# Optimization experiments

Hardware: AMD Instinct MI355X
Metric: run time of the kernel (lower is better)

Reference implementation:

```python
import jax, jax.numpy as jnp
import numpy as np

D_MODEL = 512
D_FF = 512
N_EXPERTS = 16
TOP_K = 3
BATCH, SEQ = 1, 2048


def setup_inputs() -> dict:
    key = jax.random.key(0)
    ks = jax.random.split(key, 6)
    x = jax.random.normal(ks[0], (BATCH, SEQ, D_MODEL), dtype=jnp.float32)
    # router gate (std=0.01 per _init_weights)
    gate_w = 0.01 * jax.random.normal(ks[1], (N_EXPERTS, D_MODEL), dtype=jnp.float32)
    expert_bias = jnp.zeros((N_EXPERTS,), dtype=jnp.float32)  # registered buffer, zeros
    # shared SwiGLU expert (std=0.02)
    shared_gate_up = 0.02 * jax.random.normal(ks[2], (2 * D_FF, D_MODEL), dtype=jnp.float32)
    shared_down = 0.02 * jax.random.normal(ks[3], (D_MODEL, D_FF), dtype=jnp.float32)
    # batched routed experts (std=0.02)
    expert_gate_up = 0.02 * jax.random.normal(ks[4], (N_EXPERTS, 2 * D_FF, D_MODEL), dtype=jnp.float32)
    expert_down = 0.02 * jax.random.normal(ks[5], (N_EXPERTS, D_MODEL, D_FF), dtype=jnp.float32)
    return {
        "x": x,
        "gate_w": gate_w,
        "expert_bias": expert_bias,
        "shared_gate_up": shared_gate_up,
        "shared_down": shared_down,
        "expert_gate_up": expert_gate_up,
        "expert_down": expert_down,
    }


def _swiglu(combined):
    gate, up = jnp.split(combined, 2, axis=-1)
    return jax.nn.silu(gate) * up


def reference(x, gate_w, expert_bias, shared_gate_up, shared_down, expert_gate_up, expert_down):
    B, S, D = x.shape
    xf = x.reshape(-1, D)  # [T, D]

    # ---- shared expert (always active) ----
    shared_out = _swiglu(xf @ shared_gate_up.T) @ shared_down.T  # [T, D]

    # ---- router: sigmoid affinity + bias-adjusted top-k ----
    logits = xf @ gate_w.T  # [T, E]
    affinity = jax.nn.sigmoid(logits)
    routing_scores = affinity + expert_bias  # expert_bias buffer (zeros)
    _, sel = jax.lax.top_k(routing_scores, TOP_K)  # [T, K]
    sel_aff = jnp.take_along_axis(affinity, sel, axis=1)  # [T, K]
    gating = sel_aff / (sel_aff.sum(axis=-1, keepdims=True) + 1e-9)  # [T, K]

    # ---- routed experts: per-token SwiGLU with the token's expert weights ----
    # Computed densely per expert then gathered; identical math to the
    # per-token weight-gather in BatchedExperts.
    combined = jnp.einsum('td,efd->tef', xf, expert_gate_up)  # [T, E, 2F]
    hidden = _swiglu(combined)  # [T, E, F]
    expert_out = jnp.einsum('tef,edf->ted', hidden, expert_down)  # [T, E, D]
    sel_out = jnp.take_along_axis(expert_out, sel[:, :, None], axis=1)  # [T, K, D]
    routed_out = jnp.einsum('tk,tkd->td', gating, sel_out)  # [T, D]

    out = shared_out + routed_out  # dropout p=0.0 -> identity
    return out.reshape(B, S, D)
```

## Files before the change

### kernel.cpp

```cpp
#include <hip/hip_runtime.h>

#define T_TOK 2048
#define DM    512
#define DFF   512
#define NE    16
#define LDK   72

typedef __attribute__((ext_vector_type(8))) short bf16x8;
typedef __attribute__((ext_vector_type(4))) float f32x4;
typedef __attribute__((ext_vector_type(8))) unsigned short us8;

__device__ __forceinline__ unsigned short f2bf(float f) {
  unsigned int u = __float_as_uint(f);
  u += 0x7fffu + ((u >> 16) & 1u);
  return (unsigned short)(u >> 16);
}

#define MFMA(a,b,c) __builtin_amdgcn_mfma_f32_16x16x32_bf16((a),(b),(c),0,0,0)

__global__ __launch_bounds__(256) void prep_kernel(
    const float* __restrict__ x, const float* __restrict__ gw,
    const float* __restrict__ bias, int* __restrict__ counts,
    int* __restrict__ list, float* __restrict__ wgt,
    const float* __restrict__ sgu, const float* __restrict__ sdn,
    const float* __restrict__ egu, const float* __restrict__ edn,
    unsigned short* __restrict__ xb,   unsigned short* __restrict__ sgub,
    unsigned short* __restrict__ sdnb, unsigned short* __restrict__ egub,
    unsigned short* __restrict__ ednb)
{
  const int tid = threadIdx.x;
  if (blockIdx.x >= 512) {
    int g = (blockIdx.x - 512) * 256 + tid;
    const float* s; unsigned short* d; int l;
    if      (g <  131072) { s = x;   d = xb;   l = g;           }
    else if (g <  196608) { s = sgu; d = sgub; l = g -  131072; }
    else if (g <  229376) { s = sdn; d = sdnb; l = g -  196608; }
    else if (g < 1277952) { s = egu; d = egub; l = g -  229376; }
    else                  { s = edn; d = ednb; l = g - 1277952; }
    const float* p = s + (size_t)l * 8;
    float4 v0 = *(const float4*)p;
    float4 v1 = *(const float4*)(p + 4);
    us8 o;
    o[0]=f2bf(v0.x); o[1]=f2bf(v0.y); o[2]=f2bf(v0.z); o[3]=f2bf(v0.w);
    o[4]=f2bf(v1.x); o[5]=f2bf(v1.y); o[6]=f2bf(v1.z); o[7]=f2bf(v1.w);
    *(us8*)(d + (size_t)l * 8) = o;
    return;
  }

  __shared__ float lg[4][16];
  __shared__ int bcnt[16], bbase[16];
  __shared__ int sel_s[4][3], pos_s[4][3];
  __shared__ float g_s[4][3];

  const int w = tid >> 6, lane = tid & 63;
  if (tid < 16) bcnt[tid] = 0;
  const int tok = blockIdx.x * 4 + w;
  const int e = lane & 15, part = lane >> 4;

  const float* xr = x + (size_t)tok * DM + part * 128;
  const float* wr = gw + (size_t)e * DM + part * 128;
  float acc = 0.f;
  #pragma unroll 8
  for (int i = 0; i < 128; i += 4) {
    float4 xv = *(const float4*)(xr + i);
    float4 wv = *(const float4*)(wr + i);
    acc += xv.x*wv.x + xv.y*wv.y + xv.z*wv.z + xv.w*wv.w;
  }
  acc += __shfl_xor(acc, 16);
  acc += __shfl_xor(acc, 32);
  if (lane < 16) lg[w][lane] = 1.f / (1.f + __expf(-acc));
  __syncthreads();

  if (tid < 4) {
    float aff[16], sc[16];
    #pragma unroll
    for (int i = 0; i < 16; ++i) { aff[i] = lg[tid][i]; sc[i] = aff[i] + bias[i]; }
    int sel[3]; float sa[3]; float sum = 0.f;
    #pragma unroll
    for (int k = 0; k < 3; ++k) {
      float best = -1e30f; int bi = 0;
      for (int i = 0; i < 16; ++i) {
        bool used = false;
        for (int j = 0; j < k; ++j) used |= (sel[j] == i);
        if (!used && sc[i] > best) { best = sc[i]; bi = i; }
      }
      sel[k] = bi; sa[k] = aff[bi]; sum += aff[bi];
    }
    float inv = 1.f / (sum + 1e-9f);
    #pragma unroll
    for (int k = 0; k < 3; ++k) {
      int p = atomicAdd(&bcnt[sel[k]], 1);
      sel_s[tid][k] = sel[k]; pos_s[tid][k] = p; g_s[tid][k] = sa[k] * inv;
    }
  }
  __syncthreads();
  if (tid < 16) bbase[tid] = atomicAdd(&counts[tid], bcnt[tid]);
  __syncthreads();
  if (tid < 4) {
    #pragma unroll
    for (int k = 0; k < 3; ++k) {
      int E = sel_s[tid][k];
      int p = bbase[E] + pos_s[tid][k];
      list[E * T_TOK + p] = blockIdx.x * 4 + tid;
      wgt [E * T_TOK + p] = g_s[tid][k];
    }
  }
}

__global__ __launch_bounds__(256, 4) void gemm1_fused(
    const unsigned short* __restrict__ X, const unsigned short* __restrict__ Wsh,
    const unsigned short* __restrict__ Wex, unsigned short* __restrict__ Hall,
    const int* __restrict__ counts, const int* __restrict__ list)
{
  __shared__ unsigned short As[64][LDK];
  __shared__ unsigned short Bg[64][LDK];
  __shared__ unsigned short Bu[64][LDK];

  const int n0 = blockIdx.x * 64;
  const int mt = blockIdx.y, z = blockIdx.z;
  int cnt, hb; const unsigned short* W;
  if (z == 0) { cnt = T_TOK; hb = 0; W = Wsh; }
  else {
    const int e = z - 1;
    cnt = counts[e];
    if (mt * 64 >= cnt) return;
    hb = T_TOK;
    for (int i = 0; i < e; ++i) hb += counts[i];
    W = Wex + (size_t)e * (2 * DFF * DM);
  }

  const int tid = threadIdx.x;
  const int sr = tid >> 2;
  const int sc = (tid & 3) * 16;
  const int entry = mt * 64 + sr;
  const bool avalid = entry < cnt;
  const unsigned short* arow = X;
  if (avalid) {
    const int tok = (z == 0) ? entry : list[(z - 1) * T_TOK + entry];
    arow = X + (size_t)tok * DM;
  }
  const unsigned short* grow = W + (size_t)(n0 + sr) * DM;
  const unsigned short* urow = W + (size_t)(DFF + n0 + sr) * DM;

  const int lane = tid & 63;
  const int wm = ((tid >> 6) & 1) * 32;
  const int wn = ((tid >> 7) & 1) * 32;
  const int lr = lane & 15;
  const int qd = lane >> 4;

  const f32x4 z4 = {0.f, 0.f, 0.f, 0.f};
  f32x4 accg[2][2], accu[2][2];
  #pragma unroll
  for (int i = 0; i < 2; ++i)
    #pragma unroll
    for (int j = 0; j < 2; ++j) { accg[i][j] = z4; accu[i][j] = z4; }

  for (int k0 = 0; k0 < DM; k0 += 64) {
    us8 av0 = {0,0,0,0,0,0,0,0}, av1 = {0,0,0,0,0,0,0,0};
    if (avalid) {
      av0 = *(const us8*)(arow + k0 + sc);
      av1 = *(const us8*)(arow + k0 + sc + 8);
    }
    us8 gv0 = *(const us8*)(grow + k0 + sc);
    us8 gv1 = *(const us8*)(grow + k0 + sc + 8);
    us8 uv0 = *(const us8*)(urow + k0 + sc);
    us8 uv1 = *(const us8*)(urow + k0 + sc + 8);
    __syncthreads();
    *(us8*)&As[sr][sc]     = av0; *(us8*)&As[sr][sc + 8] = av1;
    *(us8*)&Bg[sr][sc]     = gv0; *(us8*)&Bg[sr][sc + 8] = gv1;
    *(us8*)&Bu[sr][sc]     = uv0; *(us8*)&Bu[sr][sc + 8] = uv1;
    __syncthreads();
    #pragma unroll
    for (int ks = 0; ks < 2; ++ks) {
      const int kk = ks * 32 + qd * 8;
      bf16x8 a0 = *(const bf16x8*)&As[wm      + lr][kk];
      bf16x8 a1 = *(const bf16x8*)&As[wm + 16 + lr][kk];
      bf16x8 g0 = *(const bf16x8*)&Bg[wn      + lr][kk];
      bf16x8 g1 = *(const bf16x8*)&Bg[wn + 16 + lr][kk];
      bf16x8 u0 = *(const bf16x8*)&Bu[wn      + lr][kk];
      bf16x8 u1 = *(const bf16x8*)&Bu[wn + 16 + lr][kk];
      accg[0][0] = MFMA(a0, g0, accg[0][0]);
      accg[0][1] = MFMA(a0, g1, accg[0][1]);
      accg[1][0] = MFMA(a1, g0, accg[1][0]);
      accg[1][1] = MFMA(a1, g1, accg[1][1]);
      accu[0][0] = MFMA(a0, u0, accu[0][0]);
      accu[0][1] = MFMA(a0, u1, accu[0][1]);
      accu[1][0] = MFMA(a1, u0, accu[1][0]);
      accu[1][1] = MFMA(a1, u1, accu[1][1]);
    }
  }

  #pragma unroll
  for (int sm = 0; sm < 2; ++sm)
    #pragma unroll
    for (int sn = 0; sn < 2; ++sn) {
      const int col = n0 + wn + sn * 16 + lr;
      #pragma unroll
      for (int r = 0; r < 4; ++r) {
        const int ent = mt * 64 + wm + sm * 16 + qd * 4 + r;
        if (ent < cnt) {
          float g = accg[sm][sn][r];
          float u = accu[sm][sn][r];
          float h = (g / (1.f + __expf(-g))) * u;
          Hall[(size_t)(hb + ent) * DFF + col] = f2bf(h);
        }
      }
    }
}

__global__ __launch_bounds__(256, 4) void gemm2_fused(
    const unsigned short* __restrict__ Hall, const unsigned short* __restrict__ Wsh,
    const unsigned short* __restrict__ Wex, float* __restrict__ out,
    const int* __restrict__ counts, const int* __restrict__ list,
    const float* __restrict__ wgt)
{
  __shared__ unsigned short Ah[64][LDK];
  __shared__ unsigned short Bd[64][LDK];

  const int n0 = blockIdx.x * 64;
  const int mt = blockIdx.y, z = blockIdx.z;
  int cnt, hb; const unsigned short* W;
  if (z == 0) { cnt = T_TOK; hb = 0; W = Wsh; }
  else {
    const int e = z - 1;
    cnt = counts[e];
    if (mt * 64 >= cnt) return;
    hb = T_TOK;
    for (int i = 0; i < e; ++i) hb += counts[i];
    W = Wex + (size_t)e * (DM * DFF);
  }

  const int tid = threadIdx.x;
  const int sr = tid >> 2;
  const int sc = (tid & 3) * 16;
  const int entry = mt * 64 + sr;
  const bool avalid = entry < cnt;
  const unsigned short* arow = Hall;
  if (avalid) arow = Hall + (size_t)(hb + entry) * DFF;
  const unsigned short* drow = W + (size_t)(n0 + sr) * DFF;

  const int lane = tid & 63;
  const int wm = ((tid >> 6) & 1) * 32;
  const int wn = ((tid >> 7) & 1) * 32;
  const int lr = lane & 15;
  const int qd = lane >> 4;

  const f32x4 z4 = {0.f, 0.f, 0.f, 0.f};
  f32x4 acc[2][2];
  #pragma unroll
  for (int i = 0; i < 2; ++i)
    #pragma unroll
    for (int j = 0; j < 2; ++j) acc[i][j] = z4;

  for (int k0 = 0; k0 < DFF; k0 += 64) {
    us8 av0 = {0,0,0,0,0,0,0,0}, av1 = {0,0,0,0,0,0,0,0};
    if (avalid) {
      av0 = *(const us8*)(arow + k0 + sc);
      av1 = *(const us8*)(arow + k0 + sc + 8);
    }
    us8 dv0 = *(const us8*)(drow + k0 + sc);
    us8 dv1 = *(const us8*)(drow + k0 + sc + 8);
    __syncthreads();
    *(us8*)&Ah[sr][sc]     = av0; *(us8*)&Ah[sr][sc + 8] = av1;
    *(us8*)&Bd[sr][sc]     = dv0; *(us8*)&Bd[sr][sc + 8] = dv1;
    __syncthreads();
    #pragma unroll
    for (int ks = 0; ks < 2; ++ks) {
      const int kk = ks * 32 + qd * 8;
      bf16x8 a0 = *(const bf16x8*)&Ah[wm      + lr][kk];
      bf16x8 a1 = *(const bf16x8*)&Ah[wm + 16 + lr][kk];
      bf16x8 b0 = *(const bf16x8*)&Bd[wn      + lr][kk];
      bf16x8 b1 = *(const bf16x8*)&Bd[wn + 16 + lr][kk];
      acc[0][0] = MFMA(a0, b0, acc[0][0]);
      acc[0][1] = MFMA(a0, b1, acc[0][1]);
      acc[1][0] = MFMA(a1, b0, acc[1][0]);
      acc[1][1] = MFMA(a1, b1, acc[1][1]);
    }
  }

  #pragma unroll
  for (int sm = 0; sm < 2; ++sm)
    #pragma unroll
    for (int sn = 0; sn < 2; ++sn) {
      const int col = n0 + wn + sn * 16 + lr;
      #pragma unroll
      for (int r = 0; r < 4; ++r) {
        const int ent = mt * 64 + wm + sm * 16 + qd * 4 + r;
        if (ent < cnt) {
          float v = acc[sm][sn][r];
          if (z == 0) {
            atomicAdd(out + (size_t)ent * DM + col, v);
          } else {
            const int   tok = list[(z - 1) * T_TOK + ent];
            const float g   = wgt [(z - 1) * T_TOK + ent];
            atomicAdd(out + (size_t)tok * DM + col, g * v);
          }
        }
      }
    }
}

extern "C" void kernel_launch(void* const* d_in, const int* in_sizes, int n_in,
                              void* d_out, int out_size, void* d_ws, size_t ws_size,
                              hipStream_t stream) {
  const float* x    = (const float*)d_in[0];
  const float* gw   = (const float*)d_in[1];
  const float* bias = (const float*)d_in[2];
  const float* sgu  = (const float*)d_in[3];
  const float* sdn  = (const float*)d_in[4];
  const float* egu  = (const float*)d_in[5];
  const float* edn  = (const float*)d_in[6];
  float* out = (float*)d_out;

  char* ws = (char*)d_ws;
  int*            counts = (int*)(ws + 0);
  int*            list   = (int*)(ws + 64);
  float*          wgt    = (float*)(ws + 131136);
  unsigned short* Hall   = (unsigned short*)(ws + 262208);
  unsigned short* xb   = (unsigned short*)(ws + 8650816);
  unsigned short* sgub = (unsigned short*)(ws + 10747968);
  unsigned short* sdnb = (unsigned short*)(ws + 11796544);
  unsigned short* egub = (unsigned short*)(ws + 12320832);
  unsigned short* ednb = (unsigned short*)(ws + 29098048);
  const size_t need = 37486656;
  if (ws_size < need) return;

  hipMemsetAsync(counts, 0, 64, stream);
  hipMemsetAsync(out, 0, (size_t)out_size * sizeof(float), stream);

  prep_kernel<<<512 + 7040, 256, 0, stream>>>(
      x, gw, bias, counts, list, wgt, sgu, sdn, egu, edn,
      xb, sgub, sdnb, egub, ednb);
  gemm1_fused<<<dim3(8, 32, NE + 1), 256, 0, stream>>>(xb, sgub, egub, Hall, counts, list);
  gemm2_fused<<<dim3(8, 32, NE + 1), 256, 0, stream>>>(Hall, sdnb, ednb, out, counts, list, wgt);
}
```

Measured before the change: 176.6 us.

## Fuse MoE pipeline into one cooperative persistent kernel with deterministic combine

Folds bf16 conversion, routing, the gate/up GEMM, the down GEMM and the output combine into one persistent kernel, with grid-wide syncs between phases and a multi-launch fallback when cooperative launch is unavailable. Atomic scatter-adds into the output are replaced: the shared expert writes the output directly, routed results go to a staging buffer, and a final pass gathers each token's three routed rows through a token-to-slot map. This removes the extra launches, the memsets and the atomic contention. In exchange it adds grid-sync overhead, caps the grid at 1024 blocks, and spends extra memory traffic on the staging buffer.

```diff
diff --git a/kernel.cpp b/kernel.cpp
--- a/kernel.cpp
+++ b/kernel.cpp
@@ -1,4 +1,7 @@
 #include <hip/hip_runtime.h>
+#include <hip/hip_cooperative_groups.h>
+
+namespace cg = cooperative_groups;
 
 #define T_TOK 2048
 #define DM    512
@@ -18,286 +21,310 @@
 
 #define MFMA(a,b,c) __builtin_amdgcn_mfma_f32_16x16x32_bf16((a),(b),(c),0,0,0)
 
-__global__ __launch_bounds__(256) void prep_kernel(
-    const float* __restrict__ x, const float* __restrict__ gw,
-    const float* __restrict__ bias, int* __restrict__ counts,
-    int* __restrict__ list, float* __restrict__ wgt,
+__global__ __launch_bounds__(256, 4) void moe_kernel(
+    const float* __restrict__ x,   const float* __restrict__ gw,
+    const float* __restrict__ bias,
     const float* __restrict__ sgu, const float* __restrict__ sdn,
     const float* __restrict__ egu, const float* __restrict__ edn,
+    int* __restrict__ counts, int* __restrict__ list,
+    float* __restrict__ wgt,  int* __restrict__ tokslot,
     unsigned short* __restrict__ xb,   unsigned short* __restrict__ sgub,
     unsigned short* __restrict__ sdnb, unsigned short* __restrict__ egub,
-    unsigned short* __restrict__ ednb)
+    unsigned short* __restrict__ ednb,
+    unsigned short* __restrict__ Hall, float* __restrict__ ro,
+    float* __restrict__ out, int mode)
 {
-  const int tid = threadIdx.x;
-  if (blockIdx.x >= 512) {
-    int g = (blockIdx.x - 512) * 256 + tid;
-    const float* s; unsigned short* d; int l;
-    if      (g <  131072) { s = x;   d = xb;   l = g;           }
-    else if (g <  196608) { s = sgu; d = sgub; l = g -  131072; }
-    else if (g <  229376) { s = sdn; d = sdnb; l = g -  196608; }
-    else if (g < 1277952) { s = egu; d = egub; l = g -  229376; }
-    else                  { s = edn; d = ednb; l = g - 1277952; }
-    const float* p = s + (size_t)l * 8;
-    float4 v0 = *(const float4*)p;
-    float4 v1 = *(const float4*)(p + 4);
-    us8 o;
-    o[0]=f2bf(v0.x); o[1]=f2bf(v0.y); o[2]=f2bf(v0.z); o[3]=f2bf(v0.w);
-    o[4]=f2bf(v1.x); o[5]=f2bf(v1.y); o[6]=f2bf(v1.z); o[7]=f2bf(v1.w);
-    *(us8*)(d + (size_t)l * 8) = o;
-    return;
-  }
-
+  cg::grid_group gg = cg::this_grid();
+  __shared__ unsigned short SA[64][LDK];
+  __shared__ unsigned short SB[64][LDK];
+  __shared__ unsigned short SC[64][LDK];
   __shared__ float lg[4][16];
   __shared__ int bcnt[16], bbase[16];
   __shared__ int sel_s[4][3], pos_s[4][3];
   __shared__ float g_s[4][3];
-
-  const int w = tid >> 6, lane = tid & 63;
-  if (tid < 16) bcnt[tid] = 0;
-  const int tok = blockIdx.x * 4 + w;
-  const int e = lane & 15, part = lane >> 4;
-
-  const float* xr = x + (size_t)tok * DM + part * 128;
-  const float* wr = gw + (size_t)e * DM + part * 128;
-  float acc = 0.f;
-  #pragma unroll 8
-  for (int i = 0; i < 128; i += 4) {
-    float4 xv = *(const float4*)(xr + i);
-    float4 wv = *(const float4*)(wr + i);
-    acc += xv.x*wv.x + xv.y*wv.y + xv.z*wv.z + xv.w*wv.w;
-  }
-  acc += __shfl_xor(acc, 16);
-  acc += __shfl_xor(acc, 32);
-  if (lane < 16) lg[w][lane] = 1.f / (1.f + __expf(-acc));
-  __syncthreads();
-
-  if (tid < 4) {
-    float aff[16], sc[16];
-    #pragma unroll
-    for (int i = 0; i < 16; ++i) { aff[i] = lg[tid][i]; sc[i] = aff[i] + bias[i]; }
-    int sel[3]; float sa[3]; float sum = 0.f;
-    #pragma unroll
-    for (int k = 0; k < 3; ++k) {
-      float best = -1e30f; int bi = 0;
-      for (int i = 0; i < 16; ++i) {
-        bool used = false;
-        for (int j = 0; j < k; ++j) used |= (sel[j] == i);
-        if (!used && sc[i] > best) { best = sc[i]; bi = i; }
-      }
-      sel[k] = bi; sa[k] = aff[bi]; sum += aff[bi];
-    }
-    float inv = 1.f / (sum + 1e-9f);
-    #pragma unroll
-    for (int k = 0; k < 3; ++k) {
-      int p = atomicAdd(&bcnt[sel[k]], 1);
-      sel_s[tid][k] = sel[k]; pos_s[tid][k] = p; g_s[tid][k] = sa[k] * inv;
-    }
-  }
-  __syncthreads();
-  if (tid < 16) bbase[tid] = atomicAdd(&counts[tid], bcnt[tid]);
-  __syncthreads();
-  if (tid < 4) {
-    #pragma unroll
-    for (int k = 0; k < 3; ++k) {
-      int E = sel_s[tid][k];
-      int p = bbase[E] + pos_s[tid][k];
-      list[E * T_TOK + p] = blockIdx.x * 4 + tid;
-      wgt [E * T_TOK + p] = g_s[tid][k];
-    }
-  }
-}
-
-__global__ __launch_bounds__(256, 4) void gemm1_fused(
-    const unsigned short* __restrict__ X, const unsigned short* __restrict__ Wsh,
-    const unsigned short* __restrict__ Wex, unsigned short* __restrict__ Hall,
-    const int* __restrict__ counts, const int* __restrict__ list)
-{
-  __shared__ unsigned short As[64][LDK];
-  __shared__ unsigned short Bg[64][LDK];
-  __shared__ unsigned short Bu[64][LDK];
-
-  const int n0 = blockIdx.x * 64;
-  const int mt = blockIdx.y, z = blockIdx.z;
-  int cnt, hb; const unsigned short* W;
-  if (z == 0) { cnt = T_TOK; hb = 0; W = Wsh; }
-  else {
-    const int e = z - 1;
-    cnt = counts[e];
-    if (mt * 64 >= cnt) return;
-    hb = T_TOK;
-    for (int i = 0; i < e; ++i) hb += counts[i];
-    W = Wex + (size_t)e * (2 * DFF * DM);
-  }
-
-  const int tid = threadIdx.x;
-  const int sr = tid >> 2;
-  const int sc = (tid & 3) * 16;
-  const int entry = mt * 64 + sr;
-  const bool avalid = entry < cnt;
-  const unsigned short* arow = X;
-  if (avalid) {
-    const int tok = (z == 0) ? entry : list[(z - 1) * T_TOK + entry];
-    arow = X + (size_t)tok * DM;
-  }
-  const unsigned short* grow = W + (size_t)(n0 + sr) * DM;
-  const unsigned short* urow = W + (size_t)(DFF + n0 + sr) * DM;
-
-  const int lane = tid & 63;
-  const int wm = ((tid >> 6) & 1) * 32;
-  const int wn = ((tid >> 7) & 1) * 32;
-  const int lr = lane & 15;
-  const int qd = lane >> 4;
-
-  const f32x4 z4 = {0.f, 0.f, 0.f, 0.f};
-  f32x4 accg[2][2], accu[2][2];
-  #pragma unroll
-  for (int i = 0; i < 2; ++i)
-    #pragma unroll
-    for (int j = 0; j < 2; ++j) { accg[i][j] = z4; accu[i][j] = z4; }
-
-  for (int k0 = 0; k0 < DM; k0 += 64) {
-    us8 av0 = {0,0,0,0,0,0,0,0}, av1 = {0,0,0,0,0,0,0,0};
-    if (avalid) {
-      av0 = *(const us8*)(arow + k0 + sc);
-      av1 = *(const us8*)(arow + k0 + sc + 8);
-    }
-    us8 gv0 = *(const us8*)(grow + k0 + sc);
-    us8 gv1 = *(const us8*)(grow + k0 + sc + 8);
-    us8 uv0 = *(const us8*)(urow + k0 + sc);
-    us8 uv1 = *(const us8*)(urow + k0 + sc + 8);
+  __shared__ int rbase[16];
+
+  const int tid  = threadIdx.x;
+  const int nb   = gridDim.x;
+  const int gtid = blockIdx.x * 256 + tid;
+  const int T    = nb * 256;
+
+  if (mode == 0 || mode == 1) {
+    if (gtid < 16) counts[gtid] = 0;
+    for (int g = gtid; g < 1802240; g += T) {
+      const float* s; unsigned short* d; int l;
+      if      (g <  131072) { s = x;   d = xb;   l = g;           }
+      else if (g <  196608) { s = sgu; d = sgub; l = g -  131072; }
+      else if (g <  229376) { s = sdn; d = sdnb; l = g -  196608; }
+      else if (g < 1277952) { s = egu; d = egub; l = g -  229376; }
+      else                  { s = edn; d = ednb; l = g - 1277952; }
+      const float* p = s + (size_t)l * 8;
+      float4 v0 = *(const float4*)p;
+      float4 v1 = *(const float4*)(p + 4);
+      us8 o;
+      o[0]=f2bf(v0.x); o[1]=f2bf(v0.y); o[2]=f2bf(v0.z); o[3]=f2bf(v0.w);
+      o[4]=f2bf(v1.x); o[5]=f2bf(v1.y); o[6]=f2bf(v1.z); o[7]=f2bf(v1.w);
+      *(us8*)(d + (size_t)l * 8) = o;
+    }
+  }
+  if (mode == 0) gg.sync();
+
+  if (mode == 0 || mode == 2) {
+    for (int ru = blockIdx.x; ru < 512; ru += nb) {
+      const int w = tid >> 6, lane = tid & 63;
+      if (tid < 16) bcnt[tid] = 0;
+      const int tok = ru * 4 + w;
+      const int e = lane & 15, part = lane >> 4;
+
+      const float* xr = x + (size_t)tok * DM + part * 128;
+      const float* wr = gw + (size_t)e * DM + part * 128;
+      float acc = 0.f;
+      #pragma unroll 8
+      for (int i = 0; i < 128; i += 4) {
+        float4 xv = *(const float4*)(xr + i);
+        float4 wv = *(const float4*)(wr + i);
+        acc += xv.x*wv.x + xv.y*wv.y + xv.z*wv.z + xv.w*wv.w;
+      }
+      acc += __shfl_xor(acc, 16);
+      acc += __shfl_xor(acc, 32);
+      if (lane < 16) lg[w][lane] = 1.f / (1.f + __expf(-acc));
+      __syncthreads();
+
+      if (tid < 4) {
+        float aff[16], sc[16];
+        #pragma unroll
+        for (int i = 0; i < 16; ++i) { aff[i] = lg[tid][i]; sc[i] = aff[i] + bias[i]; }
+        int sel[3]; float sa[3]; float sum = 0.f;
+        #pragma unroll
+        for (int k = 0; k < 3; ++k) {
+          float best = -1e30f; int bi = 0;
+          for (int i = 0; i < 16; ++i) {
+            bool used = false;
+            for (int j = 0; j < k; ++j) used |= (sel[j] == i);
+            if (!used && sc[i] > best) { best = sc[i]; bi = i; }
+          }
+          sel[k] = bi; sa[k] = aff[bi]; sum += aff[bi];
+        }
+        float inv = 1.f / (sum + 1e-9f);
+        #pragma unroll
+        for (int k = 0; k < 3; ++k) {
+          int p = atomicAdd(&bcnt[sel[k]], 1);
+          sel_s[tid][k] = sel[k]; pos_s[tid][k] = p; g_s[tid][k] = sa[k] * inv;
+        }
+      }
+      __syncthreads();
+      if (tid < 16) bbase[tid] = atomicAdd(&counts[tid], bcnt[tid]);
+      __syncthreads();
+      if (tid < 4) {
+        #pragma unroll
+        for (int k = 0; k < 3; ++k) {
+          int E = sel_s[tid][k];
+          int p = bbase[E] + pos_s[tid][k];
+          int t = ru * 4 + tid;
+          list[E * T_TOK + p]  = t;
+          wgt [E * T_TOK + p]  = g_s[tid][k];
+          tokslot[t * 3 + k]   = (E << 16) | p;
+        }
+      }
+      __syncthreads();
+    }
+  }
+  if (mode == 0) gg.sync();
+
+  if (mode == 0 || mode == 3) {
+    for (int u = blockIdx.x; u < 17 * 256; u += nb) {
+      const int z = u >> 8, rem = u & 255, mt = rem >> 3, n0 = (rem & 7) * 64;
+      int cnt, hb; const unsigned short* W;
+      if (z == 0) { cnt = T_TOK; hb = 0; W = sgub; }
+      else {
+        cnt = counts[z - 1];
+        if (mt * 64 >= cnt) continue;
+        hb = T_TOK;
+        for (int i = 0; i < z - 1; ++i) hb += counts[i];
+        W = egub + (size_t)(z - 1) * (2 * DFF * DM);
+      }
+
+      const int sr = tid >> 2, sc = (tid & 3) * 16;
+      const int entry = mt * 64 + sr;
+      const bool avalid = entry < cnt;
+      const unsigned short* arow = xb;
+      if (avalid) {
+        const int tok = (z == 0) ? entry : list[(z - 1) * T_TOK + entry];
+        arow = xb + (size_t)tok * DM;
+      }
+      const unsigned short* grow = W + (size_t)(n0 + sr) * DM;
+      const unsigned short* urow = W + (size_t)(DFF + n0 + sr) * DM;
+
+      const int lane = tid & 63;
+      const int wm = ((tid >> 6) & 1) * 32;
+      const int wn = ((tid >> 7) & 1) * 32;
+      const int lr = lane & 15, qd = lane >> 4;
+
+      const f32x4 z4 = {0.f, 0.f, 0.f, 0.f};
+      f32x4 accg[2][2], accu[2][2];
+      #pragma unroll
+      for (int i = 0; i < 2; ++i)
+        #pragma unroll
+        for (int j = 0; j < 2; ++j) { accg[i][j] = z4; accu[i][j] = z4; }
+
+      for (int k0 = 0; k0 < DM; k0 += 64) {
+        us8 av0 = {0,0,0,0,0,0,0,0}, av1 = {0,0,0,0,0,0,0,0};
+        if (avalid) {
+          av0 = *(const us8*)(arow + k0 + sc);
+          av1 = *(const us8*)(arow + k0 + sc + 8);
+        }
+        us8 gv0 = *(const us8*)(grow + k0 + sc);
+        us8 gv1 = *(const us8*)(grow + k0 + sc + 8);
+        us8 uv0 = *(const us8*)(urow + k0 + sc);
+        us8 uv1 = *(const us8*)(urow + k0 + sc + 8);
+        __syncthreads();
+        *(us8*)&SA[sr][sc] = av0; *(us8*)&SA[sr][sc + 8] = av1;
+        *(us8*)&SB[sr][sc] = gv0; *(us8*)&SB[sr][sc + 8] = gv1;
+        *(us8*)&SC[sr][sc] = uv0; *(us8*)&SC[sr][sc + 8] = uv1;
+        __syncthreads();
+        #pragma unroll
+        for (int ks = 0; ks < 2; ++ks) {
+          const int kk = ks * 32 + qd * 8;
+          bf16x8 a0 = *(const bf16x8*)&SA[wm      + lr][kk];
+          bf16x8 a1 = *(const bf16x8*)&SA[wm + 16 + lr][kk];
+          bf16x8 g0 = *(const bf16x8*)&SB[wn      + lr][kk];
+          bf16x8 g1 = *(const bf16x8*)&SB[wn + 16 + lr][kk];
+          bf16x8 u0 = *(const bf16x8*)&SC[wn      + lr][kk];
+          bf16x8 u1 = *(const bf16x8*)&SC[wn + 16 + lr][kk];
+          accg[0][0] = MFMA(a0, g0, accg[0][0]);
+          accg[0][1] = MFMA(a0, g1, accg[0][1]);
+          accg[1][0] = MFMA(a1, g0, accg[1][0]);
+          accg[1][1] = MFMA(a1, g1, accg[1][1]);
+          accu[0][0] = MFMA(a0, u0, accu[0][0]);
+          accu[0][1] = MFMA(a0, u1, accu[0][1]);
+          accu[1][0] = MFMA(a1, u0, accu[1][0]);
+          accu[1][1] = MFMA(a1, u1, accu[1][1]);
+        }
+      }
+
+      #pragma unroll
+      for (int sm = 0; sm < 2; ++sm)
+        #pragma unroll
+        for (int sn = 0; sn < 2; ++sn) {
+          const int col = n0 + wn + sn * 16 + lr;
+          #pragma unroll
+          for (int r = 0; r < 4; ++r) {
+            const int ent = mt * 64 + wm + sm * 16 + qd * 4 + r;
+            if (ent < cnt) {
+              float g = accg[sm][sn][r];
+              float uv = accu[sm][sn][r];
+              float h = (g / (1.f + __expf(-g))) * uv;
+              Hall[(size_t)(hb + ent) * DFF + col] = f2bf(h);
+            }
+          }
+        }
+      __syncthreads();
+    }
+  }
+  if (mode == 0) gg.sync();
+
+  if (mode == 0 || mode == 4) {
+    for (int u = blockIdx.x; u < 17 * 256; u += nb) {
+      const int z = u >> 8, rem = u & 255, mt = rem >> 3, n0 = (rem & 7) * 64;
+      int cnt, hb; const unsigned short* W;
+      if (z == 0) { cnt = T_TOK; hb = 0; W = sdnb; }
+      else {
+        cnt = counts[z - 1];
+        if (mt * 64 >= cnt) continue;
+        hb = T_TOK;
+        for (int i = 0; i < z - 1; ++i) hb += counts[i];
+        W = ednb + (size_t)(z - 1) * (DM * DFF);
+      }
+      const int rb = hb - T_TOK;
+
+      const int sr = tid >> 2, sc = (tid & 3) * 16;
+      const int entry = mt * 64 + sr;
+      const bool avalid = entry < cnt;
+      const unsigned short* arow = Hall;
+      if (avalid) arow = Hall + (size_t)(hb + entry) * DFF;
+      const unsigned short* drow = W + (size_t)(n0 + sr) * DFF;
+
+      const int lane = tid & 63;
+      const int wm = ((tid >> 6) & 1) * 32;
+      const int wn = ((tid >> 7) & 1) * 32;
+      const int lr = lane & 15, qd = lane >> 4;
+
+      const f32x4 z4 = {0.f, 0.f, 0.f, 0.f};
+      f32x4 acc[2][2];
+      #pragma unroll
+      for (int i = 0; i < 2; ++i)
+        #pragma unroll
+        for (int j = 0; j < 2; ++j) acc[i][j] = z4;
+
+      for (int k0 = 0; k0 < DFF; k0 += 64) {
+        us8 av0 = {0,0,0,0,0,0,0,0}, av1 = {0,0,0,0,0,0,0,0};
+        if (avalid) {
+          av0 = *(const us8*)(arow + k0 + sc);
+          av1 = *(const us8*)(arow + k0 + sc + 8);
+        }
+        us8 dv0 = *(const us8*)(drow + k0 + sc);
+        us8 dv1 = *(const us8*)(drow + k0 + sc + 8);
+        __syncthreads();
+        *(us8*)&SA[sr][sc] = av0; *(us8*)&SA[sr][sc + 8] = av1;
+        *(us8*)&SB[sr][sc] = dv0; *(us8*)&SB[sr][sc + 8] = dv1;
+        __syncthreads();
+        #pragma unroll
+        for (int ks = 0; ks < 2; ++ks) {
+          const int kk = ks * 32 + qd * 8;
+          bf16x8 a0 = *(const bf16x8*)&SA[wm      + lr][kk];
+          bf16x8 a1 = *(const bf16x8*)&SA[wm + 16 + lr][kk];
+          bf16x8 b0 = *(const bf16x8*)&SB[wn      + lr][kk];
+          bf16x8 b1 = *(const bf16x8*)&SB[wn + 16 + lr][kk];
+          acc[0][0] = MFMA(a0, b0, acc[0][0]);
+          acc[0][1] = MFMA(a0, b1, acc[0][1]);
+          acc[1][0] = MFMA(a1, b0, acc[1][0]);
+          acc[1][1] = MFMA(a1, b1, acc[1][1]);
+        }
+      }
+
+      #pragma unroll
+      for (int sm = 0; sm < 2; ++sm)
+        #pragma unroll
+        for (int sn = 0; sn < 2; ++sn) {
+          const int col = n0 + wn + sn * 16 + lr;
+          #pragma unroll
+          for (int r = 0; r < 4; ++r) {
+            const int ent = mt * 64 + wm + sm * 16 + qd * 4 + r;
+            if (ent < cnt) {
+              float v = acc[sm][sn][r];
+              if (z == 0) {
+                out[(size_t)ent * DM + col] = v;
+              } else {
+                const float g = wgt[(z - 1) * T_TOK + ent];
+                ro[(size_t)(rb + ent) * DM + col] = g * v;
+              }
+            }
+          }
+        }
+      __syncthreads();
+    }
+  }
+  if (mode == 0) gg.sync();
+
+  if (mode == 0 || mode == 5) {
+    if (tid == 0) {
+      int s = 0;
+      for (int e = 0; e < NE; ++e) { rbase[e] = s; s += counts[e]; }
+    }
     __syncthreads();
-    *(us8*)&As[sr][sc]     = av0; *(us8*)&As[sr][sc + 8] = av1;
-    *(us8*)&Bg[sr][sc]     = gv0; *(us8*)&Bg[sr][sc + 8] = gv1;
-    *(us8*)&Bu[sr][sc]     = uv0; *(us8*)&Bu[sr][sc + 8] = uv1;
-    __syncthreads();
-    #pragma unroll
-    for (int ks = 0; ks < 2; ++ks) {
-      const int kk = ks * 32 + qd * 8;
-      bf16x8 a0 = *(const bf16x8*)&As[wm      + lr][kk];
-      bf16x8 a1 = *(const bf16x8*)&As[wm + 16 + lr][kk];
-      bf16x8 g0 = *(const bf16x8*)&Bg[wn      + lr][kk];
-      bf16x8 g1 = *(const bf16x8*)&Bg[wn + 16 + lr][kk];
-      bf16x8 u0 = *(const bf16x8*)&Bu[wn      + lr][kk];
-      bf16x8 u1 = *(const bf16x8*)&Bu[wn + 16 + lr][kk];
-      accg[0][0] = MFMA(a0, g0, accg[0][0]);
-      accg[0][1] = MFMA(a0, g1, accg[0][1]);
-      accg[1][0] = MFMA(a1, g0, accg[1][0]);
-      accg[1][1] = MFMA(a1, g1, accg[1][1]);
-      accu[0][0] = MFMA(a0, u0, accu[0][0]);
-      accu[0][1] = MFMA(a0, u1, accu[0][1]);
-      accu[1][0] = MFMA(a1, u0, accu[1][0]);
-      accu[1][1] = MFMA(a1, u1, accu[1][1]);
-    }
-  }
-
-  #pragma unroll
-  for (int sm = 0; sm < 2; ++sm)
-    #pragma unroll
-    for (int sn = 0; sn < 2; ++sn) {
-      const int col = n0 + wn + sn * 16 + lr;
-      #pragma unroll
-      for (int r = 0; r < 4; ++r) {
-        const int ent = mt * 64 + wm + sm * 16 + qd * 4 + r;
-        if (ent < cnt) {
-          float g = accg[sm][sn][r];
-          float u = accu[sm][sn][r];
-          float h = (g / (1.f + __expf(-g))) * u;
-          Hall[(size_t)(hb + ent) * DFF + col] = f2bf(h);
-        }
-      }
-    }
-}
-
-__global__ __launch_bounds__(256, 4) void gemm2_fused(
-    const unsigned short* __restrict__ Hall, const unsigned short* __restrict__ Wsh,
-    const unsigned short* __restrict__ Wex, float* __restrict__ out,
-    const int* __restrict__ counts, const int* __restrict__ list,
-    const float* __restrict__ wgt)
-{
-  __shared__ unsigned short Ah[64][LDK];
-  __shared__ unsigned short Bd[64][LDK];
-
-  const int n0 = blockIdx.x * 64;
-  const int mt = blockIdx.y, z = blockIdx.z;
-  int cnt, hb; const unsigned short* W;
-  if (z == 0) { cnt = T_TOK; hb = 0; W = Wsh; }
-  else {
-    const int e = z - 1;
-    cnt = counts[e];
-    if (mt * 64 >= cnt) return;
-    hb = T_TOK;
-    for (int i = 0; i < e; ++i) hb += counts[i];
-    W = Wex + (size_t)e * (DM * DFF);
-  }
-
-  const int tid = threadIdx.x;
-  const int sr = tid >> 2;
-  const int sc = (tid & 3) * 16;
-  const int entry = mt * 64 + sr;
-  const bool avalid = entry < cnt;
-  const unsigned short* arow = Hall;
-  if (avalid) arow = Hall + (size_t)(hb + entry) * DFF;
-  const unsigned short* drow = W + (size_t)(n0 + sr) * DFF;
-
-  const int lane = tid & 63;
-  const int wm = ((tid >> 6) & 1) * 32;
-  const int wn = ((tid >> 7) & 1) * 32;
-  const int lr = lane & 15;
-  const int qd = lane >> 4;
-
-  const f32x4 z4 = {0.f, 0.f, 0.f, 0.f};
-  f32x4 acc[2][2];
-  #pragma unroll
-  for (int i = 0; i < 2; ++i)
-    #pragma unroll
-    for (int j = 0; j < 2; ++j) acc[i][j] = z4;
-
-  for (int k0 = 0; k0 < DFF; k0 += 64) {
-    us8 av0 = {0,0,0,0,0,0,0,0}, av1 = {0,0,0,0,0,0,0,0};
-    if (avalid) {
-      av0 = *(const us8*)(arow + k0 + sc);
-      av1 = *(const us8*)(arow + k0 + sc + 8);
-    }
-    us8 dv0 = *(const us8*)(drow + k0 + sc);
-    us8 dv1 = *(const us8*)(drow + k0 + sc + 8);
-    __syncthreads();
-    *(us8*)&Ah[sr][sc]     = av0; *(us8*)&Ah[sr][sc + 8] = av1;
-    *(us8*)&Bd[sr][sc]     = dv0; *(us8*)&Bd[sr][sc + 8] = dv1;
-    __syncthreads();
-    #pragma unroll
-    for (int ks = 0; ks < 2; ++ks) {
-      const int kk = ks * 32 + qd * 8;
-      bf16x8 a0 = *(const bf16x8*)&Ah[wm      + lr][kk];
-      bf16x8 a1 = *(const bf16x8*)&Ah[wm + 16 + lr][kk];
-      bf16x8 b0 = *(const bf16x8*)&Bd[wn      + lr][kk];
-      bf16x8 b1 = *(const bf16x8*)&Bd[wn + 16 + lr][kk];
-      acc[0][0] = MFMA(a0, b0, acc[0][0]);
-      acc[0][1] = MFMA(a0, b1, acc[0][1]);
-      acc[1][0] = MFMA(a1, b0, acc[1][0]);
-      acc[1][1] = MFMA(a1, b1, acc[1][1]);
-    }
-  }
-
-  #pragma unroll
-  for (int sm = 0; sm < 2; ++sm)
-    #pragma unroll
-    for (int sn = 0; sn < 2; ++sn) {
-      const int col = n0 + wn + sn * 16 + lr;
-      #pragma unroll
-      for (int r = 0; r < 4; ++r) {
-        const int ent = mt * 64 + wm + sm * 16 + qd * 4 + r;
-        if (ent < cnt) {
-          float v = acc[sm][sn][r];
-          if (z == 0) {
-            atomicAdd(out + (size_t)ent * DM + col, v);
-          } else {
-            const int   tok = list[(z - 1) * T_TOK + ent];
-            const float g   = wgt [(z - 1) * T_TOK + ent];
-            atomicAdd(out + (size_t)tok * DM + col, g * v);
-          }
-        }
-      }
-    }
+    for (int u4 = gtid; u4 < T_TOK * (DM / 4); u4 += T) {
+      const int t = u4 >> 7, q = u4 & 127;
+      float4 o = ((const float4*)out)[(size_t)t * 128 + q];
+      #pragma unroll
+      for (int k = 0; k < 3; ++k) {
+        const int dec = tokslot[t * 3 + k];
+        const int row = rbase[dec >> 16] + (dec & 0xffff);
+        float4 r = ((const float4*)ro)[(size_t)row * 128 + q];
+        o.x += r.x; o.y += r.y; o.z += r.z; o.w += r.w;
+      }
+      ((float4*)out)[(size_t)t * 128 + q] = o;
+    }
+  }
 }
 
 extern "C" void kernel_launch(void* const* d_in, const int* in_sizes, int n_in,
@@ -313,24 +340,49 @@
   float* out = (float*)d_out;
 
   char* ws = (char*)d_ws;
-  int*            counts = (int*)(ws + 0);
-  int*            list   = (int*)(ws + 64);
-  float*          wgt    = (float*)(ws + 131136);
-  unsigned short* Hall   = (unsigned short*)(ws + 262208);
-  unsigned short* xb   = (unsigned short*)(ws + 8650816);
-  unsigned short* sgub = (unsigned short*)(ws + 10747968);
-  unsigned short* sdnb = (unsigned short*)(ws + 11796544);
-  unsigned short* egub = (unsigned short*)(ws + 12320832);
-  unsigned short* ednb = (unsigned short*)(ws + 29098048);
-  const size_t need = 37486656;
+  int*            counts  = (int*)(ws + 0);
+  int*            list    = (int*)(ws + 64);
+  float*          wgt     = (float*)(ws + 131136);
+  int*            tokslot = (int*)(ws + 262208);
+  unsigned short* Hall    = (unsigned short*)(ws + 286784);
+  float*          ro      = (float*)(ws + 8675392);
+  unsigned short* xb      = (unsigned short*)(ws + 21258304);
+  unsigned short* sgub    = (unsigned short*)(ws + 23355456);
+  unsigned short* sdnb    = (unsigned short*)(ws + 24404032);
+  unsigned short* egub    = (unsigned short*)(ws + 24928320);
+  unsigned short* ednb    = (unsigned short*)(ws + 41705536);
+  const size_t need = 50094144;
   if (ws_size < need) return;
 
-  hipMemsetAsync(counts, 0, 64, stream);
-  hipMemsetAsync(out, 0, (size_t)out_size * sizeof(float), stream);
-
-  prep_kernel<<<512 + 7040, 256, 0, stream>>>(
-      x, gw, bias, counts, list, wgt, sgu, sdn, egu, edn,
-      xb, sgub, sdnb, egub, ednb);
-  gemm1_fused<<<dim3(8, 32, NE + 1), 256, 0, stream>>>(xb, sgub, egub, Hall, counts, list);
-  gemm2_fused<<<dim3(8, 32, NE + 1), 256, 0, stream>>>(Hall, sdnb, ednb, out, counts, list, wgt);
+  int dev = 0; hipGetDevice(&dev);
+  int coop = 0;
+  hipDeviceGetAttribute(&coop, hipDeviceAttributeCooperativeLaunch, dev);
+  int nbpm = 0;
+  hipError_t oe = hipOccupancyMaxActiveBlocksPerMultiprocessor(&nbpm, moe_kernel, 256, 0);
+  if (oe != hipSuccess || nbpm < 1) nbpm = 0;
+
+  if (coop && nbpm >= 1) {
+    int blk = nbpm > 4 ? 4 : nbpm;
+    int grid = blk * 256;
+    if (grid > 1024) grid = 1024;
+    int mode0 = 0;
+    void* args[] = {(void*)&x, (void*)&gw, (void*)&bias, (void*)&sgu, (void*)&sdn,
+                    (void*)&egu, (void*)&edn, (void*)&counts, (void*)&list,
+                    (void*)&wgt, (void*)&tokslot, (void*)&xb, (void*)&sgub,
+                    (void*)&sdnb, (void*)&egub, (void*)&ednb, (void*)&Hall,
+                    (void*)&ro, (void*)&out, (void*)&mode0};
+    hipLaunchCooperativeKernel((const void*)moe_kernel, dim3(grid), dim3(256),
+                               args, 0, stream);
+  } else {
+    moe_kernel<<<2048, 256, 0, stream>>>(x, gw, bias, sgu, sdn, egu, edn,
+        counts, list, wgt, tokslot, xb, sgub, sdnb, egub, ednb, Hall, ro, out, 1);
+    moe_kernel<<< 512, 256, 0, stream>>>(x, gw, bias, sgu, sdn, egu, edn,
+        counts, list, wgt, tokslot, xb, sgub, sdnb, egub, ednb, Hall, ro, out, 2);
+    moe_kernel<<<1088, 256, 0, stream>>>(x, gw, bias, sgu, sdn, egu, edn,
+        counts, list, wgt, tokslot, xb, sgub, sdnb, egub, ednb, Hall, ro, out, 3);
+    moe_kernel<<<1088, 256, 0, stream>>>(x, gw, bias, sgu, sdn, egu, edn,
+        counts, list, wgt, tokslot, xb, sgub, sdnb, egub, ednb, Hall, ro, out, 4);
+    moe_kernel<<<1024, 256, 0, stream>>>(x, gw, bias, sgu, sdn, egu, edn,
+        counts, list, wgt, tokslot, xb, sgub, sdnb, egub, ednb, Hall, ro, out, 5);
+  }
 }
```

Measured after the change: 519.3 us. 194% more time.

## Stage GEMM tiles with direct global-to-LDS loads and XOR swizzle, fold output memset

Applied to the files above, without the earlier changes.

Both grouped GEMM kernels now load A and B tiles with global_load_lds DMA straight into a 64x64 XOR-swizzled LDS layout. This replaces the register round trip and the padded LDS arrays, and out-of-range rows are clamped to the last valid row instead of zero-filled. The output zeroing moves from a separate hipMemsetAsync into the conversion blocks of prep_kernel, which saves one launch. The loop is still single-buffered with two barriers per k-step, so load latency is still exposed.

```diff
diff --git a/kernel.cpp b/kernel.cpp
--- a/kernel.cpp
+++ b/kernel.cpp
@@ -4,7 +4,6 @@
 #define DM    512
 #define DFF   512
 #define NE    16
-#define LDK   72
 
 typedef __attribute__((ext_vector_type(8))) short bf16x8;
 typedef __attribute__((ext_vector_type(4))) float f32x4;
@@ -15,6 +14,14 @@
   u += 0x7fffu + ((u >> 16) & 1u);
   return (unsigned short)(u >> 16);
 }
+
+__device__ __forceinline__ void dma16(const unsigned short* g, unsigned short* l) {
+  __builtin_amdgcn_global_load_lds(
+      (const __attribute__((address_space(1))) unsigned int*)g,
+      (__attribute__((address_space(3))) unsigned int*)l, 16, 0, 0);
+}
+
+#define LDSOFF(row, chunk) ((((row) << 7) + ((((chunk) ^ ((row) & 7))) << 4)))
 
 #define MFMA(a,b,c) __builtin_amdgcn_mfma_f32_16x16x32_bf16((a),(b),(c),0,0,0)
 
@@ -26,11 +33,16 @@
     const float* __restrict__ egu, const float* __restrict__ edn,
     unsigned short* __restrict__ xb,   unsigned short* __restrict__ sgub,
     unsigned short* __restrict__ sdnb, unsigned short* __restrict__ egub,
-    unsigned short* __restrict__ ednb)
+    unsigned short* __restrict__ ednb, float* __restrict__ out)
 {
   const int tid = threadIdx.x;
   if (blockIdx.x >= 512) {
-    int g = (blockIdx.x - 512) * 256 + tid;
+    const int cb = blockIdx.x - 512;
+    const int ct = cb * 256 + tid;
+    const int CT = 7040 * 256;
+    const float4 z4 = {0.f, 0.f, 0.f, 0.f};
+    for (int i = ct; i < 262144; i += CT) ((float4*)out)[i] = z4;
+    int g = ct;
     const float* s; unsigned short* d; int l;
     if      (g <  131072) { s = x;   d = xb;   l = g;           }
     else if (g <  196608) { s = sgu; d = sgub; l = g -  131072; }
@@ -112,9 +124,9 @@
     const unsigned short* __restrict__ Wex, unsigned short* __restrict__ Hall,
     const int* __restrict__ counts, const int* __restrict__ list)
 {
-  __shared__ unsigned short As[64][LDK];
-  __shared__ unsigned short Bg[64][LDK];
-  __shared__ unsigned short Bu[64][LDK];
+  __shared__ unsigned short SA[64][64];
+  __shared__ unsigned short SG[64][64];
+  __shared__ unsigned short SU[64][64];
 
   const int n0 = blockIdx.x * 64;
   const int mt = blockIdx.y, z = blockIdx.z;
@@ -129,24 +141,37 @@
     W = Wex + (size_t)e * (2 * DFF * DM);
   }
 
-  const int tid = threadIdx.x;
-  const int sr = tid >> 2;
-  const int sc = (tid & 3) * 16;
-  const int entry = mt * 64 + sr;
-  const bool avalid = entry < cnt;
-  const unsigned short* arow = X;
-  if (avalid) {
-    const int tok = (z == 0) ? entry : list[(z - 1) * T_TOK + entry];
-    arow = X + (size_t)tok * DM;
-  }
-  const unsigned short* grow = W + (size_t)(n0 + sr) * DM;
-  const unsigned short* urow = W + (size_t)(DFF + n0 + sr) * DM;
-
-  const int lane = tid & 63;
+  const int tid = threadIdx.x, w = tid >> 6, lane = tid & 63;
+  const int r0 = w * 16 + (lane >> 3);
+  const int cch = (lane & 7) ^ (r0 & 7);
+  const unsigned short* ga[2];
+  #pragma unroll
+  for (int q = 0; q < 2; ++q) {
+    int ra = mt * 64 + r0 + q * 8;
+    int rc = ra < cnt ? ra : cnt - 1;
+    int tokr = (z == 0) ? rc : list[(z - 1) * T_TOK + rc];
+    ga[q] = X + (size_t)tokr * DM + cch * 8;
+  }
+  const unsigned short *gg[2], *gu[2];
+  #pragma unroll
+  for (int q = 0; q < 2; ++q) {
+    int rb = n0 + r0 + q * 8;
+    gg[q] = W + (size_t)rb * DM + cch * 8;
+    gu[q] = W + (size_t)(DFF + rb) * DM + cch * 8;
+  }
+  unsigned short* const lA0 = &SA[w * 16][0];
+  unsigned short* const lA1 = &SA[w * 16 + 8][0];
+  unsigned short* const lG0 = &SG[w * 16][0];
+  unsigned short* const lG1 = &SG[w * 16 + 8][0];
+  unsigned short* const lU0 = &SU[w * 16][0];
+  unsigned short* const lU1 = &SU[w * 16 + 8][0];
+
   const int wm = ((tid >> 6) & 1) * 32;
   const int wn = ((tid >> 7) & 1) * 32;
-  const int lr = lane & 15;
-  const int qd = lane >> 4;
+  const int lr = lane & 15, qd = lane >> 4;
+  const char* const sa = (const char*)SA;
+  const char* const sg = (const char*)SG;
+  const char* const su = (const char*)SU;
 
   const f32x4 z4 = {0.f, 0.f, 0.f, 0.f};
   f32x4 accg[2][2], accu[2][2];
@@ -156,29 +181,20 @@
     for (int j = 0; j < 2; ++j) { accg[i][j] = z4; accu[i][j] = z4; }
 
   for (int k0 = 0; k0 < DM; k0 += 64) {
-    us8 av0 = {0,0,0,0,0,0,0,0}, av1 = {0,0,0,0,0,0,0,0};
-    if (avalid) {
-      av0 = *(const us8*)(arow + k0 + sc);
-      av1 = *(const us8*)(arow + k0 + sc + 8);
-    }
-    us8 gv0 = *(const us8*)(grow + k0 + sc);
-    us8 gv1 = *(const us8*)(grow + k0 + sc + 8);
-    us8 uv0 = *(const us8*)(urow + k0 + sc);
-    us8 uv1 = *(const us8*)(urow + k0 + sc + 8);
     __syncthreads();
-    *(us8*)&As[sr][sc]     = av0; *(us8*)&As[sr][sc + 8] = av1;
-    *(us8*)&Bg[sr][sc]     = gv0; *(us8*)&Bg[sr][sc + 8] = gv1;
-    *(us8*)&Bu[sr][sc]     = uv0; *(us8*)&Bu[sr][sc + 8] = uv1;
+    dma16(ga[0] + k0, lA0); dma16(ga[1] + k0, lA1);
+    dma16(gg[0] + k0, lG0); dma16(gg[1] + k0, lG1);
+    dma16(gu[0] + k0, lU0); dma16(gu[1] + k0, lU1);
     __syncthreads();
     #pragma unroll
     for (int ks = 0; ks < 2; ++ks) {
-      const int kk = ks * 32 + qd * 8;
-      bf16x8 a0 = *(const bf16x8*)&As[wm      + lr][kk];
-      bf16x8 a1 = *(const bf16x8*)&As[wm + 16 + lr][kk];
-      bf16x8 g0 = *(const bf16x8*)&Bg[wn      + lr][kk];
-      bf16x8 g1 = *(const bf16x8*)&Bg[wn + 16 + lr][kk];
-      bf16x8 u0 = *(const bf16x8*)&Bu[wn      + lr][kk];
-      bf16x8 u1 = *(const bf16x8*)&Bu[wn + 16 + lr][kk];
+      const int ch = ks * 4 + qd;
+      bf16x8 a0 = *(const bf16x8*)(sa + LDSOFF(wm      + lr, ch));
+      bf16x8 a1 = *(const bf16x8*)(sa + LDSOFF(wm + 16 + lr, ch));
+      bf16x8 g0 = *(const bf16x8*)(sg + LDSOFF(wn      + lr, ch));
+      bf16x8 g1 = *(const bf16x8*)(sg + LDSOFF(wn + 16 + lr, ch));
+      bf16x8 u0 = *(const bf16x8*)(su + LDSOFF(wn      + lr, ch));
+      bf16x8 u1 = *(const bf16x8*)(su + LDSOFF(wn + 16 + lr, ch));
       accg[0][0] = MFMA(a0, g0, accg[0][0]);
       accg[0][1] = MFMA(a0, g1, accg[0][1]);
       accg[1][0] = MFMA(a1, g0, accg[1][0]);
@@ -214,8 +230,8 @@
     const int* __restrict__ counts, const int* __restrict__ list,
     const float* __restrict__ wgt)
 {
-  __shared__ unsigned short Ah[64][LDK];
-  __shared__ unsigned short Bd[64][LDK];
+  __shared__ unsigned short SA[64][64];
+  __shared__ unsigned short SB[64][64];
 
   const int n0 = blockIdx.x * 64;
   const int mt = blockIdx.y, z = blockIdx.z;
@@ -230,20 +246,30 @@
     W = Wex + (size_t)e * (DM * DFF);
   }
 
-  const int tid = threadIdx.x;
-  const int sr = tid >> 2;
-  const int sc = (tid & 3) * 16;
-  const int entry = mt * 64 + sr;
-  const bool avalid = entry < cnt;
-  const unsigned short* arow = Hall;
-  if (avalid) arow = Hall + (size_t)(hb + entry) * DFF;
-  const unsigned short* drow = W + (size_t)(n0 + sr) * DFF;
-
-  const int lane = tid & 63;
+  const int tid = threadIdx.x, w = tid >> 6, lane = tid & 63;
+  const int r0 = w * 16 + (lane >> 3);
+  const int cch = (lane & 7) ^ (r0 & 7);
+  const unsigned short* ga[2];
+  #pragma unroll
+  for (int q = 0; q < 2; ++q) {
+    int ra = mt * 64 + r0 + q * 8;
+    int rc = ra < cnt ? ra : cnt - 1;
+    ga[q] = Hall + (size_t)(hb + rc) * DFF + cch * 8;
+  }
+  const unsigned short* gb[2];
+  #pragma unroll
+  for (int q = 0; q < 2; ++q)
+    gb[q] = W + (size_t)(n0 + r0 + q * 8) * DFF + cch * 8;
+  unsigned short* const lA0 = &SA[w * 16][0];
+  unsigned short* const lA1 = &SA[w * 16 + 8][0];
+  unsigned short* const lB0 = &SB[w * 16][0];
+  unsigned short* const lB1 = &SB[w * 16 + 8][0];
+
   const int wm = ((tid >> 6) & 1) * 32;
   const int wn = ((tid >> 7) & 1) * 32;
-  const int lr = lane & 15;
-  const int qd = lane >> 4;
+  const int lr = lane & 15, qd = lane >> 4;
+  const char* const sa = (const char*)SA;
+  const char* const sb = (const char*)SB;
 
   const f32x4 z4 = {0.f, 0.f, 0.f, 0.f};
   f32x4 acc[2][2];
@@ -253,24 +279,17 @@
     for (int j = 0; j < 2; ++j) acc[i][j] = z4;
 
   for (int k0 = 0; k0 < DFF; k0 += 64) {
-    us8 av0 = {0,0,0,0,0,0,0,0}, av1 = {0,0,0,0,0,0,0,0};
-    if (avalid) {
-      av0 = *(const us8*)(arow + k0 + sc);
-      av1 = *(const us8*)(arow + k0 + sc + 8);
-    }
-    us8 dv0 = *(const us8*)(drow + k0 + sc);
-    us8 dv1 = *(const us8*)(drow + k0 + sc + 8);
     __syncthreads();
-    *(us8*)&Ah[sr][sc]     = av0; *(us8*)&Ah[sr][sc + 8] = av1;
-    *(us8*)&Bd[sr][sc]     = dv0; *(us8*)&Bd[sr][sc + 8] = dv1;
+    dma16(ga[0] + k0, lA0); dma16(ga[1] + k0, lA1);
+    dma16(gb[0] + k0, lB0); dma16(gb[1] + k0, lB1);
     __syncthreads();
     #pragma unroll
     for (int ks = 0; ks < 2; ++ks) {
-      const int kk = ks * 32 + qd * 8;
-      bf16x8 a0 = *(const bf16x8*)&Ah[wm      + lr][kk];
-      bf16x8 a1 = *(const bf16x8*)&Ah[wm + 16 + lr][kk];
-      bf16x8 b0 = *(const bf16x8*)&Bd[wn      + lr][kk];
-      bf16x8 b1 = *(const bf16x8*)&Bd[wn + 16 + lr][kk];
+      const int ch = ks * 4 + qd;
+      bf16x8 a0 = *(const bf16x8*)(sa + LDSOFF(wm      + lr, ch));
+      bf16x8 a1 = *(const bf16x8*)(sa + LDSOFF(wm + 16 + lr, ch));
+      bf16x8 b0 = *(const bf16x8*)(sb + LDSOFF(wn      + lr, ch));
+      bf16x8 b1 = *(const bf16x8*)(sb + LDSOFF(wn + 16 + lr, ch));
       acc[0][0] = MFMA(a0, b0, acc[0][0]);
       acc[0][1] = MFMA(a0, b1, acc[0][1]);
       acc[1][0] = MFMA(a1, b0, acc[1][0]);
@@ -317,20 +336,18 @@
   int*            list   = (int*)(ws + 64);
   float*          wgt    = (float*)(ws + 131136);
   unsigned short* Hall   = (unsigned short*)(ws + 262208);
-  unsigned short* xb   = (unsigned short*)(ws + 8650816);
-  unsigned short* sgub = (unsigned short*)(ws + 10747968);
-  unsigned short* sdnb = (unsigned short*)(ws + 11796544);
-  unsigned short* egub = (unsigned short*)(ws + 12320832);
-  unsigned short* ednb = (unsigned short*)(ws + 29098048);
+  unsigned short* xb     = (unsigned short*)(ws + 8650816);
+  unsigned short* sgub   = (unsigned short*)(ws + 10747968);
+  unsigned short* sdnb   = (unsigned short*)(ws + 11796544);
+  unsigned short* egub   = (unsigned short*)(ws + 12320832);
+  unsigned short* ednb   = (unsigned short*)(ws + 29098048);
   const size_t need = 37486656;
   if (ws_size < need) return;
 
   hipMemsetAsync(counts, 0, 64, stream);
-  hipMemsetAsync(out, 0, (size_t)out_size * sizeof(float), stream);
-
   prep_kernel<<<512 + 7040, 256, 0, stream>>>(
       x, gw, bias, counts, list, wgt, sgu, sdn, egu, edn,
-      xb, sgub, sdnb, egub, ednb);
+      xb, sgub, sdnb, egub, ednb, out);
   gemm1_fused<<<dim3(8, 32, NE + 1), 256, 0, stream>>>(xb, sgub, egub, Hall, counts, list);
   gemm2_fused<<<dim3(8, 32, NE + 1), 256, 0, stream>>>(Hall, sdnb, ednb, out, counts, list, wgt);
 }
```

New measurement: 169.0 us. 1.04x faster.
